# Performance work log

Hardware: AMD Instinct MI355X
Metric: run time of the kernel (lower is better)

Reference implementation:

```python
import jax, jax.numpy as jnp
import numpy as np
from jax import lax


def setup_inputs() -> dict:
    key = jax.random.key(0)
    ks = jax.random.split(key, 7)
    B, S, D, E = 4, 4096, 1024, 8
    H = 4 * D
    scale = 0.02
    x = jax.random.normal(ks[0], (B, S, D), dtype=jnp.float32)
    Wg = jax.random.normal(ks[1], (D, E), dtype=jnp.float32) * scale
    bg = jnp.zeros((E,), dtype=jnp.float32)
    W1 = jax.random.normal(ks[2], (E, D, H), dtype=jnp.float32) * scale
    b1 = jnp.zeros((E, H), dtype=jnp.float32)
    W2 = jax.random.normal(ks[3], (E, H, D), dtype=jnp.float32) * scale
    b2 = jnp.zeros((E, D), dtype=jnp.float32)
    return {"x": x, "Wg": Wg, "bg": bg, "W1": W1, "b1": b1,
            "W2": W2, "b2": b2, "topk_num": 2}


def _moe_forward(x, Wg, bg, W1, b1, W2, b2, topk_num):
    B, S, D = x.shape
    E = Wg.shape[1]
    flat_x = x.reshape(-1, D)                      # (T, D)
    T = flat_x.shape[0]
    # Router: clean logits (source bug: noise computed on noisy_logits but
    # topk/softmax operate on `logits`), sparse softmax over top-k experts.
    logits = flat_x @ Wg + bg                      # (T, E)
    topk_vals, topk_idx = lax.top_k(logits, topk_num)   # (T, k)
    probs = jax.nn.softmax(topk_vals, axis=-1)     # softmax over -inf-masked == softmax over topk
    gates = jnp.zeros((T, E), dtype=x.dtype).at[
        jnp.arange(T)[:, None], topk_idx].set(probs)    # (T, E), 0 for unrouted
    # Dispatch/compute/combine: gate weight is exactly 0 for unrouted tokens,
    # so a dense per-expert FFN weighted by the gate matches the masked
    # gather-FFN-scatter math of the original.
    out = jnp.zeros_like(flat_x)
    for e in range(E):
        h = jax.nn.relu(flat_x @ W1[e] + b1[e])    # (T, 4D)
        y = h @ W2[e] + b2[e]                      # (T, D)
        out = out + gates[:, e:e + 1] * y
    return out.reshape(B, S, D)


def reference(x, Wg, bg, W1, b1, W2, b2, topk_num):
    return _moe_forward(x, Wg, bg, W1, b1, W2, b2, topk_num)
```

## Files before the change

### kernel.cpp

```cpp
#include <hip/hip_runtime.h>
#include <cstdint>
#include <cstddef>

typedef unsigned short u16;
typedef __bf16 bf16x8 __attribute__((ext_vector_type(8)));
typedef u16    u16x8  __attribute__((ext_vector_type(8)));
typedef float  f32x4  __attribute__((ext_vector_type(4)));

static __device__ __forceinline__ u16 f2bf(float f) {
  uint32_t u = __builtin_bit_cast(uint32_t, f);
  u += 0x7FFFu + ((u >> 16) & 1u);
  return (u16)(u >> 16);
}
static __device__ __forceinline__ float bf2f(u16 h) {
  return __builtin_bit_cast(float, (uint32_t)h << 16);
}
static __device__ __forceinline__ bf16x8 as_bf(u16x8 v) {
  union { u16x8 u; bf16x8 b; } x; x.u = v; return x.b;
}

#define GLD_LDS(src, dst)                                                      \
  __builtin_amdgcn_global_load_lds(                                            \
      (const __attribute__((address_space(1))) void*)(const void*)(src),       \
      (__attribute__((address_space(3))) void*)(void*)(dst), 16, 0, 0)

#define T_TOK 16384
#define DDIM  1024
#define EEXP  8
#define HDIM  4096
#define BM    128
#define MAXTILES 264
#define MAXSLOTS 33792

__global__ __launch_bounds__(256) void transpose_cast(
    const float* __restrict__ in, u16* __restrict__ out, int R, int C) {
  __shared__ float t[32][33];
  int e = blockIdx.z;
  const float* src = in + (size_t)e * R * C;
  u16* dst = out + (size_t)e * R * C;
  int c0 = blockIdx.x * 32, r0 = blockIdx.y * 32;
  int tx = threadIdx.x & 31, ty = threadIdx.x >> 5;
#pragma unroll
  for (int i = 0; i < 4; i++)
    t[ty + i * 8][tx] = src[(size_t)(r0 + ty + i * 8) * C + c0 + tx];
  __syncthreads();
#pragma unroll
  for (int i = 0; i < 4; i++)
    dst[(size_t)(c0 + ty + i * 8) * R + r0 + tx] = f2bf(t[tx][ty + i * 8]);
}

__global__ __launch_bounds__(256) void router_kernel(
    const float* __restrict__ x, const float* __restrict__ Wg,
    const float* __restrict__ bg, u16* __restrict__ xbf,
    int2* __restrict__ tok_e, float2* __restrict__ tok_g,
    int* __restrict__ counts) {
  int w = threadIdx.x >> 6, lane = threadIdx.x & 63;
  int t = blockIdx.x * 4 + w;
  const float* xr = x + (size_t)t * DDIM;
  float acc[EEXP] = {0.f, 0.f, 0.f, 0.f, 0.f, 0.f, 0.f, 0.f};
#pragma unroll
  for (int j = 0; j < DDIM / 64; j++) {
    int d = j * 64 + lane;
    float xv = xr[d];
    xbf[(size_t)t * DDIM + d] = f2bf(xv);
    const float4* wv = (const float4*)(Wg + (size_t)d * EEXP);
    float4 wa = wv[0], wb = wv[1];
    acc[0] += xv * wa.x; acc[1] += xv * wa.y;
    acc[2] += xv * wa.z; acc[3] += xv * wa.w;
    acc[4] += xv * wb.x; acc[5] += xv * wb.y;
    acc[6] += xv * wb.z; acc[7] += xv * wb.w;
  }
#pragma unroll
  for (int e = 0; e < EEXP; e++) {
    float v = acc[e];
    for (int s = 32; s; s >>= 1) v += __shfl_xor(v, s);
    acc[e] = v + bg[e];
  }
  int e0 = 0; float v0 = acc[0];
#pragma unroll
  for (int e = 1; e < EEXP; e++) if (acc[e] > v0) { v0 = acc[e]; e0 = e; }
  int e1 = -1; float v1 = -3.402823466e38f;
#pragma unroll
  for (int e = 0; e < EEXP; e++)
    if (e != e0 && acc[e] > v1) { v1 = acc[e]; e1 = e; }
  float p0 = 1.f / (1.f + expf(v1 - v0));
  float p1 = 1.f - p0;
  if (lane == 0) {
    atomicAdd(&counts[e0], 1);
    atomicAdd(&counts[e1], 1);
    tok_e[t] = make_int2(e0, e1);
    tok_g[t] = make_float2(p0, p1);
  }
}

__global__ void scan_kernel(const int* __restrict__ counts,
                            int* __restrict__ expBase,
                            int* __restrict__ tileExpert,
                            int* __restrict__ tileRow0,
                            int* __restrict__ nTiles) {
  if (threadIdx.x != 0 || blockIdx.x != 0) return;
  int base = 0, nt = 0;
  for (int e = 0; e < EEXP; e++) {
    expBase[e] = base;
    int c = counts[e];
    int tiles = (c + BM - 1) >> 7;
    for (int i = 0; i < tiles; i++) {
      tileExpert[nt] = e;
      tileRow0[nt] = base + i * BM;
      nt++;
    }
    base += tiles << 7;
  }
  *nTiles = nt;
}

__global__ __launch_bounds__(256) void scatter_kernel(
    const int2* __restrict__ tok_e, int* __restrict__ cursor,
    const int* __restrict__ expBase, int* __restrict__ rowmap,
    int2* __restrict__ tokslot) {
  int t = blockIdx.x * 256 + threadIdx.x;
  int2 e = tok_e[t];
  int s0 = expBase[e.x] + atomicAdd(&cursor[e.x], 1);
  int s1 = expBase[e.y] + atomicAdd(&cursor[e.y], 1);
  rowmap[s0] = t;
  rowmap[s1] = t;
  tokslot[t] = make_int2(s0, s1);
}

template <bool RELU, bool GATHER>
__global__ __launch_bounds__(256) void moe_gemm(
    const u16* __restrict__ A,
    const u16* __restrict__ Bt,
    const float* __restrict__ bias,
    u16* __restrict__ C,
    const int* __restrict__ rowmap,
    const int* __restrict__ tileExpert, const int* __restrict__ tileRow0,
    const int* __restrict__ nTiles, int N, int K) {
  __shared__ __align__(16) u16 As[BM * 64];
  __shared__ __align__(16) u16 Bs[BM * 64];
  int nt = N >> 7;
  int mtile = (int)blockIdx.x / nt;
  if (mtile >= *nTiles) return;
  int ntile = (int)blockIdx.x % nt;
  int e = tileExpert[mtile];
  int row0 = tileRow0[mtile];
  const u16* Bm = Bt + (size_t)e * N * K;
  const float* bb = bias + (size_t)e * N;
  int ncol0 = ntile << 7;

  int tid = threadIdx.x, lane = tid & 63, w = tid >> 6;
  int wr = w >> 1, wc = w & 1;

  const u16* asrc[4];
  const u16* bsrc[4];
#pragma unroll
  for (int j = 0; j < 4; j++) {
    int cc = (w * 4 + j) * 64 + lane;
    int row = cc >> 3, kc = cc & 7;
    int slot = row0 + row;
    int ar = GATHER ? rowmap[slot] : slot;
    asrc[j] = A + (size_t)ar * K + kc * 8;
    bsrc[j] = Bm + (size_t)(ncol0 + row) * K + kc * 8;
  }

  f32x4 acc[4][4] = {};

  for (int k0 = 0; k0 < K; k0 += 64) {
    __syncthreads();
#pragma unroll
    for (int j = 0; j < 4; j++)
      GLD_LDS(asrc[j] + k0, &As[(w * 4 + j) * 512]);
#pragma unroll
    for (int j = 0; j < 4; j++)
      GLD_LDS(bsrc[j] + k0, &Bs[(w * 4 + j) * 512]);
    __syncthreads();
#pragma unroll
    for (int kk = 0; kk < 64; kk += 32) {
      u16x8 av[4], bv[4];
#pragma unroll
      for (int m = 0; m < 4; m++)
        av[m] = *reinterpret_cast<const u16x8*>(
            &As[(wr * 64 + m * 16 + (lane & 15)) * 64 + kk + (lane >> 4) * 8]);
#pragma unroll
      for (int n = 0; n < 4; n++)
        bv[n] = *reinterpret_cast<const u16x8*>(
            &Bs[(wc * 64 + n * 16 + (lane & 15)) * 64 + kk + (lane >> 4) * 8]);
#pragma unroll
      for (int m = 0; m < 4; m++)
#pragma unroll
        for (int n = 0; n < 4; n++)
          acc[m][n] = __builtin_amdgcn_mfma_f32_16x16x32_bf16(
              as_bf(av[m]), as_bf(bv[n]), acc[m][n], 0, 0, 0);
    }
  }

  int r4 = (lane >> 4) * 4;
  int cl = lane & 15;
#pragma unroll
  for (int m = 0; m < 4; m++) {
    int rbase = row0 + wr * 64 + m * 16 + r4;
#pragma unroll
    for (int n = 0; n < 4; n++) {
      int col = ncol0 + wc * 64 + n * 16 + cl;
      float bval = bb[col];
#pragma unroll
      for (int j = 0; j < 4; j++) {
        float v = acc[m][n][j] + bval;
        if (RELU) v = fmaxf(v, 0.f);
        C[(size_t)(rbase + j) * N + col] = f2bf(v);
      }
    }
  }
}

__global__ __launch_bounds__(256) void combine_kernel(
    const u16* __restrict__ Y, const int2* __restrict__ tokslot,
    const float2* __restrict__ tok_g, float* __restrict__ out) {
  int gid = blockIdx.x * 256 + threadIdx.x;
  int t = gid >> 7, seg = (gid & 127) * 8;
  int2 s = tokslot[t];
  float2 g = tok_g[t];
  u16x8 y0 = *reinterpret_cast<const u16x8*>(Y + (size_t)s.x * DDIM + seg);
  u16x8 y1 = *reinterpret_cast<const u16x8*>(Y + (size_t)s.y * DDIM + seg);
  float* op = out + (size_t)t * DDIM + seg;
#pragma unroll
  for (int i = 0; i < 8; i++)
    op[i] = g.x * bf2f(y0[i]) + g.y * bf2f(y1[i]);
}

extern "C" void kernel_launch(void* const* d_in, const int* in_sizes, int n_in,
                              void* d_out, int out_size, void* d_ws,
                              size_t ws_size, hipStream_t stream) {
  (void)in_sizes; (void)n_in; (void)out_size; (void)ws_size;
  const float* x  = (const float*)d_in[0];
  const float* Wg = (const float*)d_in[1];
  const float* bg = (const float*)d_in[2];
  const float* W1 = (const float*)d_in[3];
  const float* b1 = (const float*)d_in[4];
  const float* W2 = (const float*)d_in[5];
  const float* b2 = (const float*)d_in[6];
  float* out = (float*)d_out;

  char* ws = (char*)d_ws;
  size_t o = 0;
  u16* W1T = (u16*)(ws + o); o += (size_t)EEXP * DDIM * HDIM * 2;
  u16* W2T = (u16*)(ws + o); o += (size_t)EEXP * HDIM * DDIM * 2;
  u16* xbf = (u16*)(ws + o); o += (size_t)T_TOK * DDIM * 2;
  u16* Hbuf = (u16*)(ws + o); o += (size_t)MAXSLOTS * HDIM * 2;
  u16* Ybuf = (u16*)(ws + o); o += (size_t)MAXSLOTS * DDIM * 2;
  int* rowmap = (int*)(ws + o); o += (size_t)MAXSLOTS * 4;
  int2* tok_e = (int2*)(ws + o); o += (size_t)T_TOK * 8;
  float2* tok_g = (float2*)(ws + o); o += (size_t)T_TOK * 8;
  int2* tokslot = (int2*)(ws + o); o += (size_t)T_TOK * 8;
  int* counts = (int*)(ws + o); o += 8 * 4;
  int* cursor = (int*)(ws + o); o += 8 * 4;
  int* expBase = (int*)(ws + o); o += 8 * 4;
  int* nTiles = (int*)(ws + o); o += 8 * 4;
  int* tileExpert = (int*)(ws + o); o += MAXTILES * 4;
  int* tileRow0 = (int*)(ws + o); o += MAXTILES * 4;

  hipMemsetAsync(counts, 0, 16 * 4, stream);
  hipMemsetAsync(rowmap, 0, (size_t)MAXSLOTS * 4, stream);

  transpose_cast<<<dim3(HDIM / 32, DDIM / 32, EEXP), 256, 0, stream>>>(W1, W1T, DDIM, HDIM);
  transpose_cast<<<dim3(DDIM / 32, HDIM / 32, EEXP), 256, 0, stream>>>(W2, W2T, HDIM, DDIM);

  router_kernel<<<T_TOK / 4, 256, 0, stream>>>(x, Wg, bg, xbf, tok_e, tok_g, counts);
  scan_kernel<<<1, 64, 0, stream>>>(counts, expBase, tileExpert, tileRow0, nTiles);
  scatter_kernel<<<T_TOK / 256, 256, 0, stream>>>(tok_e, cursor, expBase, rowmap, tokslot);

  moe_gemm<true, true><<<MAXTILES * (HDIM / 128), 256, 0, stream>>>(
      xbf, W1T, b1, Hbuf, rowmap, tileExpert, tileRow0, nTiles, HDIM, DDIM);
  moe_gemm<false, false><<<MAXTILES * (DDIM / 128), 256, 0, stream>>>(
      Hbuf, W2T, b2, Ybuf, nullptr, tileExpert, tileRow0, nTiles, DDIM, HDIM);

  combine_kernel<<<(T_TOK * (DDIM / 8)) / 256, 256, 0, stream>>>(Ybuf, tokslot, tok_g, out);
}
```

Measured before the change: 1.910 ms.

## Use 256x256 double-buffered MoE GEMM with swizzled LDS and fused atomic combine

Replaces the 128x128 grouped GEMM with a 256x256-tile, 512-thread kernel. It double-buffers LDS, XOR-swizzles the LDS layout, staggers the prefetch between phases, raises wave priority around the MFMAs and remaps block IDs. The second GEMM now applies the gate weights and scatters into the output with float atomics, which removes the Y buffer and the combine kernel. The weight transpose-cast uses 64x64 tiles with vectorized loads and stores. The risks are more padded rows per expert, atomic contention on the output, a high LDS footprint per block, and run-to-run nondeterministic summation order.

Result: slower. 2.011 ms (+5.3%).

```diff
diff --git a/kernel.cpp b/kernel.cpp
--- a/kernel.cpp
+++ b/kernel.cpp
@@ -28,25 +28,38 @@
 #define DDIM  1024
 #define EEXP  8
 #define HDIM  4096
-#define BM    128
-#define MAXTILES 264
-#define MAXSLOTS 33792
-
-__global__ __launch_bounds__(256) void transpose_cast(
+#define BM256 256
+#define MAXTILES 136
+#define MAXSLOTS 34816
+
+__global__ __launch_bounds__(256) void transpose_cast64(
     const float* __restrict__ in, u16* __restrict__ out, int R, int C) {
-  __shared__ float t[32][33];
+  __shared__ float t[64][65];
   int e = blockIdx.z;
   const float* src = in + (size_t)e * R * C;
   u16* dst = out + (size_t)e * R * C;
-  int c0 = blockIdx.x * 32, r0 = blockIdx.y * 32;
-  int tx = threadIdx.x & 31, ty = threadIdx.x >> 5;
-#pragma unroll
-  for (int i = 0; i < 4; i++)
-    t[ty + i * 8][tx] = src[(size_t)(r0 + ty + i * 8) * C + c0 + tx];
+  int r0 = blockIdx.y << 6, c0 = blockIdx.x << 6;
+  int tr = threadIdx.x >> 4;
+  int tc = (threadIdx.x & 15) << 2;
+#pragma unroll
+  for (int i = 0; i < 4; i++) {
+    const float4 v = *(const float4*)(src + (size_t)(r0 + tr + i * 16) * C + c0 + tc);
+    t[tr + i * 16][tc + 0] = v.x;
+    t[tr + i * 16][tc + 1] = v.y;
+    t[tr + i * 16][tc + 2] = v.z;
+    t[tr + i * 16][tc + 3] = v.w;
+  }
   __syncthreads();
-#pragma unroll
-  for (int i = 0; i < 4; i++)
-    dst[(size_t)(c0 + ty + i * 8) * R + r0 + tx] = f2bf(t[tx][ty + i * 8]);
+  int oc = threadIdx.x >> 3;
+  int rr = (threadIdx.x & 7) << 3;
+#pragma unroll
+  for (int i = 0; i < 2; i++) {
+    int c = oc + (i << 5);
+    u16x8 o;
+#pragma unroll
+    for (int j = 0; j < 8; j++) o[j] = f2bf(t[rr + j][c]);
+    *(u16x8*)(dst + (size_t)(c0 + c) * R + r0 + rr) = o;
+  }
 }
 
 __global__ __launch_bounds__(256) void router_kernel(
@@ -103,13 +116,13 @@
   for (int e = 0; e < EEXP; e++) {
     expBase[e] = base;
     int c = counts[e];
-    int tiles = (c + BM - 1) >> 7;
+    int tiles = (c + BM256 - 1) >> 8;
     for (int i = 0; i < tiles; i++) {
       tileExpert[nt] = e;
-      tileRow0[nt] = base + i * BM;
+      tileRow0[nt] = base + (i << 8);
       nt++;
     }
-    base += tiles << 7;
+    base += tiles << 8;
   }
   *nTiles = nt;
 }
@@ -117,121 +130,202 @@
 __global__ __launch_bounds__(256) void scatter_kernel(
     const int2* __restrict__ tok_e, int* __restrict__ cursor,
     const int* __restrict__ expBase, int* __restrict__ rowmap,
-    int2* __restrict__ tokslot) {
+    float* __restrict__ gateOf, const float2* __restrict__ tok_g) {
   int t = blockIdx.x * 256 + threadIdx.x;
   int2 e = tok_e[t];
+  float2 g = tok_g[t];
   int s0 = expBase[e.x] + atomicAdd(&cursor[e.x], 1);
   int s1 = expBase[e.y] + atomicAdd(&cursor[e.y], 1);
   rowmap[s0] = t;
   rowmap[s1] = t;
-  tokslot[t] = make_int2(s0, s1);
-}
-
-template <bool RELU, bool GATHER>
-__global__ __launch_bounds__(256) void moe_gemm(
+  gateOf[s0] = g.x;
+  gateOf[s1] = g.y;
+}
+
+template <bool RELU_STORE, bool GATHER, bool ATOMIC_OUT>
+__global__ __launch_bounds__(512) void moe_gemm256(
     const u16* __restrict__ A,
     const u16* __restrict__ Bt,
     const float* __restrict__ bias,
-    u16* __restrict__ C,
-    const int* __restrict__ rowmap,
+    u16* __restrict__ Cbf,
+    float* __restrict__ Cout,
+    const float* __restrict__ gateOf, const int* __restrict__ rowmap,
     const int* __restrict__ tileExpert, const int* __restrict__ tileRow0,
     const int* __restrict__ nTiles, int N, int K) {
-  __shared__ __align__(16) u16 As[BM * 64];
-  __shared__ __align__(16) u16 Bs[BM * 64];
-  int nt = N >> 7;
-  int mtile = (int)blockIdx.x / nt;
+  __shared__ __align__(16) u16 As[2][256 * 64];
+  __shared__ __align__(16) u16 Bs[2][256 * 64];
+  int ntl = N >> 8;
+  int nwg = (int)gridDim.x;
+  int bid = (int)blockIdx.x;
+  int swzb = (bid & 7) * (nwg >> 3) + (bid >> 3);
+  int mtile = swzb / ntl, ntile = swzb - mtile * ntl;
   if (mtile >= *nTiles) return;
-  int ntile = (int)blockIdx.x % nt;
   int e = tileExpert[mtile];
   int row0 = tileRow0[mtile];
+  int ncol0 = ntile << 8;
   const u16* Bm = Bt + (size_t)e * N * K;
   const float* bb = bias + (size_t)e * N;
-  int ncol0 = ntile << 7;
-
-  int tid = threadIdx.x, lane = tid & 63, w = tid >> 6;
-  int wr = w >> 1, wc = w & 1;
-
-  const u16* asrc[4];
-  const u16* bsrc[4];
+
+  int tid = threadIdx.x;
+  int wv = tid >> 6, lane = tid & 63;
+  int wr = wv >> 2, wc = wv & 3;
+  int rlo = lane & 15, hi = lane >> 4;
+
+  int srow = tid >> 3;
+  int gkc = (tid & 7) ^ (srow & 7);
+  const u16* asrc[4]; const u16* bsrc[4];
 #pragma unroll
   for (int j = 0; j < 4; j++) {
-    int cc = (w * 4 + j) * 64 + lane;
-    int row = cc >> 3, kc = cc & 7;
-    int slot = row0 + row;
-    int ar = GATHER ? rowmap[slot] : slot;
-    asrc[j] = A + (size_t)ar * K + kc * 8;
-    bsrc[j] = Bm + (size_t)(ncol0 + row) * K + kc * 8;
-  }
-
-  f32x4 acc[4][4] = {};
-
-  for (int k0 = 0; k0 < K; k0 += 64) {
-    __syncthreads();
-#pragma unroll
-    for (int j = 0; j < 4; j++)
-      GLD_LDS(asrc[j] + k0, &As[(w * 4 + j) * 512]);
-#pragma unroll
-    for (int j = 0; j < 4; j++)
-      GLD_LDS(bsrc[j] + k0, &Bs[(w * 4 + j) * 512]);
-    __syncthreads();
-#pragma unroll
-    for (int kk = 0; kk < 64; kk += 32) {
-      u16x8 av[4], bv[4];
-#pragma unroll
-      for (int m = 0; m < 4; m++)
-        av[m] = *reinterpret_cast<const u16x8*>(
-            &As[(wr * 64 + m * 16 + (lane & 15)) * 64 + kk + (lane >> 4) * 8]);
-#pragma unroll
-      for (int n = 0; n < 4; n++)
-        bv[n] = *reinterpret_cast<const u16x8*>(
-            &Bs[(wc * 64 + n * 16 + (lane & 15)) * 64 + kk + (lane >> 4) * 8]);
-#pragma unroll
-      for (int m = 0; m < 4; m++)
-#pragma unroll
-        for (int n = 0; n < 4; n++)
-          acc[m][n] = __builtin_amdgcn_mfma_f32_16x16x32_bf16(
-              as_bf(av[m]), as_bf(bv[n]), acc[m][n], 0, 0, 0);
-    }
-  }
-
-  int r4 = (lane >> 4) * 4;
-  int cl = lane & 15;
-#pragma unroll
-  for (int m = 0; m < 4; m++) {
-    int rbase = row0 + wr * 64 + m * 16 + r4;
-#pragma unroll
-    for (int n = 0; n < 4; n++) {
-      int col = ncol0 + wc * 64 + n * 16 + cl;
-      float bval = bb[col];
+    int row = j * 64 + srow;
+    int ar = GATHER ? rowmap[row0 + row] : (row0 + row);
+    asrc[j] = A + (size_t)ar * K + gkc * 8;
+    bsrc[j] = Bm + (size_t)(ncol0 + row) * K + gkc * 8;
+  }
+
+  f32x4 acc[8][4] = {};
+  int nkt = K >> 6;
+
+#pragma unroll
+  for (int j = 0; j < 4; j++) GLD_LDS(asrc[j], &As[0][j * 4096 + wv * 512]);
+#pragma unroll
+  for (int j = 0; j < 4; j++) GLD_LDS(bsrc[j], &Bs[0][j * 4096 + wv * 512]);
+
+  int swA0 = ((hi + 0) ^ (rlo & 7)) * 8;
+  int swA4 = ((hi + 4) ^ (rlo & 7)) * 8;
+
+  for (int kt = 0; kt < nkt; ++kt) {
+    const u16* as = As[kt & 1];
+    const u16* bs = Bs[kt & 1];
+    u16* an = As[(kt & 1) ^ 1];
+    u16* bn = Bs[(kt & 1) ^ 1];
+    int sk = (kt + 1) << 6;
+    bool pf = (kt + 1 < nkt);
+
+    asm volatile("s_waitcnt vmcnt(0)" ::: "memory");
+    __builtin_amdgcn_s_barrier();
+    __builtin_amdgcn_sched_barrier(0);
+
+    u16x8 af[4][2], b0[2][2], b1[2][2];
+    if (pf) {
+#pragma unroll
+      for (int j = 0; j < 4; j++) GLD_LDS(asrc[j] + sk, &an[j * 4096 + wv * 512]);
+    }
+#pragma unroll
+    for (int m = 0; m < 4; m++) {
+      int rb = (wr * 128 + m * 16 + rlo) * 64;
+      af[m][0] = *(const u16x8*)(as + rb + swA0);
+      af[m][1] = *(const u16x8*)(as + rb + swA4);
+    }
+#pragma unroll
+    for (int n = 0; n < 2; n++) {
+      int rb = (wc * 64 + n * 16 + rlo) * 64;
+      b0[n][0] = *(const u16x8*)(bs + rb + swA0);
+      b0[n][1] = *(const u16x8*)(bs + rb + swA4);
+    }
+    __builtin_amdgcn_s_setprio(1);
+#pragma unroll
+    for (int m = 0; m < 4; m++)
+#pragma unroll
+      for (int n = 0; n < 2; n++) {
+        acc[m][n] = __builtin_amdgcn_mfma_f32_16x16x32_bf16(as_bf(af[m][0]), as_bf(b0[n][0]), acc[m][n], 0, 0, 0);
+        acc[m][n] = __builtin_amdgcn_mfma_f32_16x16x32_bf16(as_bf(af[m][1]), as_bf(b0[n][1]), acc[m][n], 0, 0, 0);
+      }
+    __builtin_amdgcn_s_setprio(0);
+    __builtin_amdgcn_s_barrier();
+
+    if (pf) {
+#pragma unroll
+      for (int j = 0; j < 4; j++) GLD_LDS(bsrc[j] + sk, &bn[j * 4096 + wv * 512]);
+    }
+#pragma unroll
+    for (int n = 0; n < 2; n++) {
+      int rb = (wc * 64 + (n + 2) * 16 + rlo) * 64;
+      b1[n][0] = *(const u16x8*)(bs + rb + swA0);
+      b1[n][1] = *(const u16x8*)(bs + rb + swA4);
+    }
+    __builtin_amdgcn_s_setprio(1);
+#pragma unroll
+    for (int m = 0; m < 4; m++)
+#pragma unroll
+      for (int n = 0; n < 2; n++) {
+        acc[m][n + 2] = __builtin_amdgcn_mfma_f32_16x16x32_bf16(as_bf(af[m][0]), as_bf(b1[n][0]), acc[m][n + 2], 0, 0, 0);
+        acc[m][n + 2] = __builtin_amdgcn_mfma_f32_16x16x32_bf16(as_bf(af[m][1]), as_bf(b1[n][1]), acc[m][n + 2], 0, 0, 0);
+      }
+    __builtin_amdgcn_s_setprio(0);
+    __builtin_amdgcn_s_barrier();
+
+#pragma unroll
+    for (int m = 0; m < 4; m++) {
+      int rb = (wr * 128 + (m + 4) * 16 + rlo) * 64;
+      af[m][0] = *(const u16x8*)(as + rb + swA0);
+      af[m][1] = *(const u16x8*)(as + rb + swA4);
+    }
+    __builtin_amdgcn_s_setprio(1);
+#pragma unroll
+    for (int m = 0; m < 4; m++)
+#pragma unroll
+      for (int n = 0; n < 2; n++) {
+        acc[m + 4][n + 2] = __builtin_amdgcn_mfma_f32_16x16x32_bf16(as_bf(af[m][0]), as_bf(b1[n][0]), acc[m + 4][n + 2], 0, 0, 0);
+        acc[m + 4][n + 2] = __builtin_amdgcn_mfma_f32_16x16x32_bf16(as_bf(af[m][1]), as_bf(b1[n][1]), acc[m + 4][n + 2], 0, 0, 0);
+      }
+    __builtin_amdgcn_s_setprio(0);
+    __builtin_amdgcn_s_barrier();
+
+    __builtin_amdgcn_s_setprio(1);
+#pragma unroll
+    for (int m = 0; m < 4; m++)
+#pragma unroll
+      for (int n = 0; n < 2; n++) {
+        acc[m + 4][n] = __builtin_amdgcn_mfma_f32_16x16x32_bf16(as_bf(af[m][0]), as_bf(b0[n][0]), acc[m + 4][n], 0, 0, 0);
+        acc[m + 4][n] = __builtin_amdgcn_mfma_f32_16x16x32_bf16(as_bf(af[m][1]), as_bf(b0[n][1]), acc[m + 4][n], 0, 0, 0);
+      }
+    __builtin_amdgcn_s_setprio(0);
+  }
+
+  asm volatile("s_waitcnt vmcnt(0)" ::: "memory");
+  int r4 = hi * 4;
+  if (!ATOMIC_OUT) {
+#pragma unroll
+    for (int m = 0; m < 8; m++) {
+      int rb = row0 + wr * 128 + m * 16 + r4;
+#pragma unroll
+      for (int n = 0; n < 4; n++) {
+        int col = ncol0 + wc * 64 + n * 16 + rlo;
+        float bv = bb[col];
+#pragma unroll
+        for (int j = 0; j < 4; j++) {
+          float v = acc[m][n][j] + bv;
+          if (RELU_STORE) v = fmaxf(v, 0.f);
+          Cbf[(size_t)(rb + j) * N + col] = f2bf(v);
+        }
+      }
+    }
+  } else {
+#pragma unroll
+    for (int m = 0; m < 8; m++) {
+      int rb = row0 + wr * 128 + m * 16 + r4;
 #pragma unroll
       for (int j = 0; j < 4; j++) {
-        float v = acc[m][n][j] + bval;
-        if (RELU) v = fmaxf(v, 0.f);
-        C[(size_t)(rbase + j) * N + col] = f2bf(v);
-      }
-    }
-  }
-}
-
-__global__ __launch_bounds__(256) void combine_kernel(
-    const u16* __restrict__ Y, const int2* __restrict__ tokslot,
-    const float2* __restrict__ tok_g, float* __restrict__ out) {
-  int gid = blockIdx.x * 256 + threadIdx.x;
-  int t = gid >> 7, seg = (gid & 127) * 8;
-  int2 s = tokslot[t];
-  float2 g = tok_g[t];
-  u16x8 y0 = *reinterpret_cast<const u16x8*>(Y + (size_t)s.x * DDIM + seg);
-  u16x8 y1 = *reinterpret_cast<const u16x8*>(Y + (size_t)s.y * DDIM + seg);
-  float* op = out + (size_t)t * DDIM + seg;
-#pragma unroll
-  for (int i = 0; i < 8; i++)
-    op[i] = g.x * bf2f(y0[i]) + g.y * bf2f(y1[i]);
+        int slot = rb + j;
+        float g = gateOf[slot];
+        if (g != 0.f) {
+          int t = rowmap[slot];
+          float* op = Cout + (size_t)t * DDIM;
+#pragma unroll
+          for (int n = 0; n < 4; n++) {
+            int col = ncol0 + wc * 64 + n * 16 + rlo;
+            atomicAdd(op + col, g * (acc[m][n][j] + bb[col]));
+          }
+        }
+      }
+    }
+  }
 }
 
 extern "C" void kernel_launch(void* const* d_in, const int* in_sizes, int n_in,
                               void* d_out, int out_size, void* d_ws,
                               size_t ws_size, hipStream_t stream) {
-  (void)in_sizes; (void)n_in; (void)out_size; (void)ws_size;
+  (void)in_sizes; (void)n_in; (void)ws_size;
   const float* x  = (const float*)d_in[0];
   const float* Wg = (const float*)d_in[1];
   const float* bg = (const float*)d_in[2];
@@ -247,11 +341,10 @@
   u16* W2T = (u16*)(ws + o); o += (size_t)EEXP * HDIM * DDIM * 2;
   u16* xbf = (u16*)(ws + o); o += (size_t)T_TOK * DDIM * 2;
   u16* Hbuf = (u16*)(ws + o); o += (size_t)MAXSLOTS * HDIM * 2;
-  u16* Ybuf = (u16*)(ws + o); o += (size_t)MAXSLOTS * DDIM * 2;
   int* rowmap = (int*)(ws + o); o += (size_t)MAXSLOTS * 4;
+  float* gateOf = (float*)(ws + o); o += (size_t)MAXSLOTS * 4;
   int2* tok_e = (int2*)(ws + o); o += (size_t)T_TOK * 8;
   float2* tok_g = (float2*)(ws + o); o += (size_t)T_TOK * 8;
-  int2* tokslot = (int2*)(ws + o); o += (size_t)T_TOK * 8;
   int* counts = (int*)(ws + o); o += 8 * 4;
   int* cursor = (int*)(ws + o); o += 8 * 4;
   int* expBase = (int*)(ws + o); o += 8 * 4;
@@ -261,18 +354,18 @@
 
   hipMemsetAsync(counts, 0, 16 * 4, stream);
   hipMemsetAsync(rowmap, 0, (size_t)MAXSLOTS * 4, stream);
-
-  transpose_cast<<<dim3(HDIM / 32, DDIM / 32, EEXP), 256, 0, stream>>>(W1, W1T, DDIM, HDIM);
-  transpose_cast<<<dim3(DDIM / 32, HDIM / 32, EEXP), 256, 0, stream>>>(W2, W2T, HDIM, DDIM);
+  hipMemsetAsync(gateOf, 0, (size_t)MAXSLOTS * 4, stream);
+  hipMemsetAsync(out, 0, (size_t)out_size * 4, stream);
+
+  transpose_cast64<<<dim3(HDIM / 64, DDIM / 64, EEXP), 256, 0, stream>>>(W1, W1T, DDIM, HDIM);
+  transpose_cast64<<<dim3(DDIM / 64, HDIM / 64, EEXP), 256, 0, stream>>>(W2, W2T, HDIM, DDIM);
 
   router_kernel<<<T_TOK / 4, 256, 0, stream>>>(x, Wg, bg, xbf, tok_e, tok_g, counts);
   scan_kernel<<<1, 64, 0, stream>>>(counts, expBase, tileExpert, tileRow0, nTiles);
-  scatter_kernel<<<T_TOK / 256, 256, 0, stream>>>(tok_e, cursor, expBase, rowmap, tokslot);
-
-  moe_gemm<true, true><<<MAXTILES * (HDIM / 128), 256, 0, stream>>>(
-      xbf, W1T, b1, Hbuf, rowmap, tileExpert, tileRow0, nTiles, HDIM, DDIM);
-  moe_gemm<false, false><<<MAXTILES * (DDIM / 128), 256, 0, stream>>>(
-      Hbuf, W2T, b2, Ybuf, nullptr, tileExpert, tileRow0, nTiles, DDIM, HDIM);
-
-  combine_kernel<<<(T_TOK * (DDIM / 8)) / 256, 256, 0, stream>>>(Ybuf, tokslot, tok_g, out);
-}
+  scatter_kernel<<<T_TOK / 256, 256, 0, stream>>>(tok_e, cursor, expBase, rowmap, gateOf, tok_g);
+
+  moe_gemm256<true, true, false><<<MAXTILES * (HDIM / 256), 512, 0, stream>>>(
+      xbf, W1T, b1, Hbuf, nullptr, nullptr, rowmap, tileExpert, tileRow0, nTiles, HDIM, DDIM);
+  moe_gemm256<false, false, true><<<MAXTILES * (DDIM / 256), 512, 0, stream>>>(
+      Hbuf, W2T, b2, nullptr, out, gateOf, rowmap, tileExpert, tileRow0, nTiles, DDIM, HDIM);
+}
```
